# Optimization experiments

Hardware: AMD Instinct MI355X
Metric: run time of the kernel (lower is better)

## Reference

```python
import jax, jax.numpy as jnp
import numpy as np

N, E, D, K = 32768, 16384, 4, 8          # nodes, hyperedges, edges/node, nodes/edge
IN_DIM, OUT_DIM, EDGE_DIM, NUM_HEADS = 128, 128, 64, 8


def setup_inputs() -> dict:
    key = jax.random.key(0)
    ks = jax.random.split(key, 16)
    s_in = 1.0 / np.sqrt(IN_DIM)
    s_out = 1.0 / np.sqrt(OUT_DIM)
    s_edge = 1.0 / np.sqrt(EDGE_DIM)
    return {
        "x": jax.random.normal(ks[0], (N, IN_DIM), jnp.float32),
        "edge_attr": jax.random.normal(ks[1], (E, EDGE_DIM), jnp.float32),
        "node_edges": jax.random.randint(ks[2], (N, D), 0, E),   # hyperedges containing each node
        "edge_nodes": jax.random.randint(ks[3], (E, K), 0, N),   # nodes inside each hyperedge
        "W_lin": jax.random.normal(ks[4], (OUT_DIM, IN_DIM), jnp.float32) * s_in,
        "W_edge": jax.random.normal(ks[5], (OUT_DIM, EDGE_DIM), jnp.float32) * s_edge,
        "Wq": jax.random.normal(ks[6], (OUT_DIM, OUT_DIM), jnp.float32) * s_out,
        "Wk": jax.random.normal(ks[7], (OUT_DIM, OUT_DIM), jnp.float32) * s_out,
        "Wv": jax.random.normal(ks[8], (OUT_DIM, OUT_DIM), jnp.float32) * s_out,
        "bq": jnp.zeros((OUT_DIM,), jnp.float32),
        "bk": jnp.zeros((OUT_DIM,), jnp.float32),
        "bv": jnp.zeros((OUT_DIM,), jnp.float32),
        "Wo": jax.random.normal(ks[9], (OUT_DIM, OUT_DIM), jnp.float32) * s_out,
        "bo": jnp.zeros((OUT_DIM,), jnp.float32),
    }


def reference(x, edge_attr, node_edges, edge_nodes,
              W_lin, W_edge, Wq, Wk, Wv, bq, bk, bv, Wo, bo):
    n, out_dim = x.shape[0], W_lin.shape[0]
    hd = out_dim // NUM_HEADS
    L = node_edges.shape[1] * edge_nodes.shape[1]  # D*K keys per node

    Wh = x @ W_lin.T                               # [N, out]
    We = edge_attr @ W_edge.T                      # [E, out]

    u_idx = edge_nodes[node_edges]                 # [N, D, K] neighbor node ids
    vals = Wh[u_idx]                               # [N, D, K, out]
    keys = vals + We[node_edges][:, :, None, :]    # key = Wh[u] + We[e]
    keys = keys.reshape(n, L, out_dim)
    vals = vals.reshape(n, L, out_dim)

    # torch nn.MultiheadAttention: single query per node (query = Wh[v])
    q = (Wh @ Wq.T + bq).reshape(n, NUM_HEADS, hd)
    k = (keys @ Wk.T + bk).reshape(n, L, NUM_HEADS, hd)
    v = (vals @ Wv.T + bv).reshape(n, L, NUM_HEADS, hd)

    scores = jnp.einsum('nhd,nlhd->nhl', q, k) / jnp.sqrt(jnp.asarray(hd, q.dtype))
    attn = jax.nn.softmax(scores, axis=-1)         # [N, H, L]
    ctx = jnp.einsum('nhl,nlhd->nhd', attn, v).reshape(n, out_dim)
    out = ctx @ Wo.T + bo
    return jax.nn.relu(out)
```

## Files before the change

### kernel.cpp

```cpp
#include <hip/hip_runtime.h>

#define N_NODES 32768
#define N_EDGES 16384
#define DEG 4
#define KPE 8
#define DIM 128
#define EDIM 64

typedef float f32x4 __attribute__((ext_vector_type(4)));
typedef __bf16 bf16x8 __attribute__((ext_vector_type(8)));
typedef __bf16 bf16x2 __attribute__((ext_vector_type(2)));
typedef unsigned short u16x8 __attribute__((ext_vector_type(8)));
typedef unsigned int u32;

static __device__ __forceinline__ unsigned short f2bf(float f) {
  union { float f; unsigned int u; } v; v.f = f;
  unsigned int r = (v.u + 0x7FFFu + ((v.u >> 16) & 1u)) >> 16;
  return (unsigned short)r;
}
static __device__ __forceinline__ float bflo(unsigned int v) {
  union { unsigned int u; float f; } x; x.u = v << 16; return x.f;
}
static __device__ __forceinline__ float bfhi(unsigned int v) {
  union { unsigned int u; float f; } x; x.u = v & 0xffff0000u; return x.f;
}

#if __has_builtin(__builtin_amdgcn_fdot2_f32_bf16)
static __device__ __forceinline__ float dot2bf(unsigned int a, unsigned int b, float c) {
  return __builtin_amdgcn_fdot2_f32_bf16(
      __builtin_bit_cast(bf16x2, a), __builtin_bit_cast(bf16x2, b), c, false);
}
#else
static __device__ __forceinline__ float dot2bf(unsigned int a, unsigned int b, float c) {
  c = fmaf(bflo(a), bflo(b), c);
  return fmaf(bfhi(a), bfhi(b), c);
}
#endif

__global__ __launch_bounds__(256) void wprep_kernel(
    const float* __restrict__ Wq, const float* __restrict__ Wk,
    const float* __restrict__ Wv, const float* __restrict__ Wlin,
    const float* __restrict__ Wedge, const float* __restrict__ Wo,
    unsigned short* __restrict__ CW, unsigned short* __restrict__ CWE,
    unsigned short* __restrict__ Wob)
{
  int id = blockIdx.x * 256 + threadIdx.x;
  if (id < 384 * 128) {
    int j = id >> 7, i = id & 127;
    const float* wrow; float scale = 1.0f;
    if (j < 128)      { wrow = Wq + j * 128; scale = 0.25f; }
    else if (j < 256) { wrow = Wk + (j - 128) * 128; }
    else              { wrow = Wv + (j - 256) * 128; }
    float s = 0.f;
    #pragma unroll 8
    for (int m = 0; m < 128; ++m) s += wrow[m] * Wlin[m * 128 + i];
    CW[id] = f2bf(s * scale);
  } else if (id < 384 * 128 + 128 * 64) {
    int id2 = id - 384 * 128; int j = id2 >> 6, t = id2 & 63;
    float s = 0.f;
    #pragma unroll 8
    for (int m = 0; m < 128; ++m) s += Wk[j * 128 + m] * Wedge[m * 64 + t];
    CWE[id2] = f2bf(s);
  } else if (id < 384 * 128 + 128 * 64 + 128 * 128) {
    int id3 = id - (384 * 128 + 128 * 64);
    Wob[id3] = f2bf(Wo[id3]);
  }
}

__global__ __launch_bounds__(256) void g1_kernel(
    const float* __restrict__ x, const unsigned short* __restrict__ CW,
    const float* __restrict__ bq, const float* __restrict__ bv,
    unsigned short* __restrict__ qb, unsigned short* __restrict__ Kb,
    unsigned short* __restrict__ Vb)
{
  const int wave = threadIdx.x >> 6, lane = threadIdx.x & 63;
  const int r16 = lane & 15, quad = lane >> 4;
  const int m0 = blockIdx.x * 64 + wave * 16;

  u16x8 av[4];
  const float* arow = x + (size_t)(m0 + r16) * DIM + quad * 8;
  #pragma unroll
  for (int kk = 0; kk < 4; ++kk) {
    float4 a0 = *(const float4*)(arow + kk * 32);
    float4 a1 = *(const float4*)(arow + kk * 32 + 4);
    u16x8 au;
    au[0] = f2bf(a0.x); au[1] = f2bf(a0.y); au[2] = f2bf(a0.z); au[3] = f2bf(a0.w);
    au[4] = f2bf(a1.x); au[5] = f2bf(a1.y); au[6] = f2bf(a1.z); au[7] = f2bf(a1.w);
    av[kk] = au;
  }

  #pragma unroll
  for (int g = 0; g < 6; ++g) {
    f32x4 acc[4];
    const f32x4 z = {0.f, 0.f, 0.f, 0.f};
    acc[0] = z; acc[1] = z; acc[2] = z; acc[3] = z;
    #pragma unroll
    for (int kk = 0; kk < 4; ++kk) {
      #pragma unroll
      for (int s = 0; s < 4; ++s) {
        u16x8 bu = *(const u16x8*)(CW + (size_t)(g * 64 + s * 16 + r16) * DIM + kk * 32 + quad * 8);
        acc[s] = __builtin_amdgcn_mfma_f32_16x16x32_bf16(
            __builtin_bit_cast(bf16x8, av[kk]), __builtin_bit_cast(bf16x8, bu), acc[s], 0, 0, 0);
      }
    }
    const int arr = g >> 1;
    const int colbase = (g & 1) * 64;
    unsigned short* dst = arr == 0 ? qb : (arr == 1 ? Kb : Vb);
    #pragma unroll
    for (int s = 0; s < 4; ++s) {
      int j = colbase + s * 16 + r16;
      float bias = arr == 0 ? 0.25f * bq[j] : (arr == 2 ? bv[j] : 0.f);
      #pragma unroll
      for (int r = 0; r < 4; ++r) {
        int m = m0 + quad * 4 + r;
        dst[(size_t)m * DIM + j] = f2bf(acc[s][r] + bias);
      }
    }
  }
}

__global__ __launch_bounds__(256) void g2_kernel(
    const float* __restrict__ ea, const unsigned short* __restrict__ CWE,
    const float* __restrict__ bk, unsigned short* __restrict__ WeKb)
{
  const int wave = threadIdx.x >> 6, lane = threadIdx.x & 63;
  const int r16 = lane & 15, quad = lane >> 4;
  const int m0 = blockIdx.x * 64 + wave * 16;
  const int n0 = blockIdx.y * 64;

  f32x4 acc[4];
  const f32x4 z = {0.f, 0.f, 0.f, 0.f};
  acc[0] = z; acc[1] = z; acc[2] = z; acc[3] = z;

  const float* arow = ea + (size_t)(m0 + r16) * EDIM + quad * 8;
  #pragma unroll
  for (int kk = 0; kk < 2; ++kk) {
    float4 a0 = *(const float4*)(arow + kk * 32);
    float4 a1 = *(const float4*)(arow + kk * 32 + 4);
    u16x8 au;
    au[0] = f2bf(a0.x); au[1] = f2bf(a0.y); au[2] = f2bf(a0.z); au[3] = f2bf(a0.w);
    au[4] = f2bf(a1.x); au[5] = f2bf(a1.y); au[6] = f2bf(a1.z); au[7] = f2bf(a1.w);
    bf16x8 av = __builtin_bit_cast(bf16x8, au);
    #pragma unroll
    for (int s = 0; s < 4; ++s) {
      u16x8 bu = *(const u16x8*)(CWE + (size_t)(n0 + s * 16 + r16) * EDIM + kk * 32 + quad * 8);
      acc[s] = __builtin_amdgcn_mfma_f32_16x16x32_bf16(
          av, __builtin_bit_cast(bf16x8, bu), acc[s], 0, 0, 0);
    }
  }

  #pragma unroll
  for (int s = 0; s < 4; ++s) {
    int j = n0 + s * 16 + r16;
    float bias = bk[j];
    #pragma unroll
    for (int r = 0; r < 4; ++r) {
      int m = m0 + quad * 4 + r;
      WeKb[(size_t)m * DIM + j] = f2bf(acc[s][r] + bias);
    }
  }
}

__global__ __launch_bounds__(64, 2) void attn_kernel(
    const unsigned short* __restrict__ qb, const unsigned short* __restrict__ Kb,
    const unsigned short* __restrict__ Vb, const unsigned short* __restrict__ WeKb,
    const int* __restrict__ nedges, const int* __restrict__ enodes,
    unsigned short* __restrict__ ctxb)
{
  __shared__ __align__(16) unsigned short ldsV[32][128];
  __shared__ __align__(16) float ldsP[8][36];
  const int lane = threadIdx.x;
  const int n = blockIdx.x;
  const int l = lane & 31, half = lane >> 5;
  const int j = l >> 3, lo8 = l & 7;
  const int c0 = lane * 2;
  const int h = lane >> 3;

  int4 e4 = *(const int4*)(nedges + (size_t)n * DEG);
  int e = (j & 2) ? ((j & 1) ? e4.w : e4.z) : ((j & 1) ? e4.y : e4.x);
  int u = enodes[(size_t)e * KPE + lo8];

  int4 m0 = *(const int4*)(enodes + (size_t)e4.x * KPE);
  int4 m1 = *(const int4*)(enodes + (size_t)e4.x * KPE + 4);
  int4 m2 = *(const int4*)(enodes + (size_t)e4.y * KPE);
  int4 m3 = *(const int4*)(enodes + (size_t)e4.y * KPE + 4);
  int4 m4 = *(const int4*)(enodes + (size_t)e4.z * KPE);
  int4 m5 = *(const int4*)(enodes + (size_t)e4.z * KPE + 4);
  int4 m6 = *(const int4*)(enodes + (size_t)e4.w * KPE);
  int4 m7 = *(const int4*)(enodes + (size_t)e4.w * KPE + 4);

  const uint4* qp = (const uint4*)(qb + (size_t)n * DIM + half * 64);
  const uint4* kp = (const uint4*)(Kb + (size_t)u * DIM + half * 64);
  const uint4* ep = (const uint4*)(WeKb + (size_t)e * DIM + half * 64);
  uint4 qv[8], kv[8], ev[8];
  #pragma unroll
  for (int ch = 0; ch < 8; ++ch) qv[ch] = qp[ch];
  #pragma unroll
  for (int ch = 0; ch < 8; ++ch) kv[ch] = kp[ch];
  #pragma unroll
  for (int ch = 0; ch < 8; ++ch) ev[ch] = ep[ch];

#define STAGE_V(t, node) do {                                                   \
    const u32* gp_ = (const u32*)(Vb + (size_t)(node) * DIM) + lane;            \
    __builtin_amdgcn_global_load_lds(                                           \
        (const __attribute__((address_space(1))) u32*)gp_,                      \
        (__attribute__((address_space(3))) u32*)&ldsV[t][0], 4, 0, 0);          \
  } while (0)
  STAGE_V(0,  m0.x); STAGE_V(1,  m0.y); STAGE_V(2,  m0.z); STAGE_V(3,  m0.w);
  STAGE_V(4,  m1.x); STAGE_V(5,  m1.y); STAGE_V(6,  m1.z); STAGE_V(7,  m1.w);
  STAGE_V(8,  m2.x); STAGE_V(9,  m2.y); STAGE_V(10, m2.z); STAGE_V(11, m2.w);
  STAGE_V(12, m3.x); STAGE_V(13, m3.y); STAGE_V(14, m3.z); STAGE_V(15, m3.w);
  STAGE_V(16, m4.x); STAGE_V(17, m4.y); STAGE_V(18, m4.z); STAGE_V(19, m4.w);
  STAGE_V(20, m5.x); STAGE_V(21, m5.y); STAGE_V(22, m5.z); STAGE_V(23, m5.w);
  STAGE_V(24, m6.x); STAGE_V(25, m6.y); STAGE_V(26, m6.z); STAGE_V(27, m6.w);
  STAGE_V(28, m7.x); STAGE_V(29, m7.y); STAGE_V(30, m7.z); STAGE_V(31, m7.w);
#undef STAGE_V

  float s[4] = {0.f, 0.f, 0.f, 0.f};
  #pragma unroll
  for (int ch = 0; ch < 8; ++ch) {
    const int hi = ch >> 1;
    float t = s[hi];
    t = dot2bf(qv[ch].x, kv[ch].x, t); t = dot2bf(qv[ch].x, ev[ch].x, t);
    t = dot2bf(qv[ch].y, kv[ch].y, t); t = dot2bf(qv[ch].y, ev[ch].y, t);
    t = dot2bf(qv[ch].z, kv[ch].z, t); t = dot2bf(qv[ch].z, ev[ch].z, t);
    t = dot2bf(qv[ch].w, kv[ch].w, t); t = dot2bf(qv[ch].w, ev[ch].w, t);
    s[hi] = t;
  }

  #pragma unroll
  for (int hi = 0; hi < 4; ++hi) {
    float vmax = s[hi];
    #pragma unroll
    for (int off = 16; off >= 1; off >>= 1)
      vmax = fmaxf(vmax, __shfl_xor(vmax, off, 32));
    float ex = __expf(s[hi] - vmax);
    float sum = ex;
    #pragma unroll
    for (int off = 16; off >= 1; off >>= 1)
      sum += __shfl_xor(sum, off, 32);
    ldsP[half * 4 + hi][l] = ex / sum;
  }
  __syncthreads();

  float a0 = 0.f, a1 = 0.f;
  #pragma unroll
  for (int t = 0; t < 8; ++t) {
    float4 p4 = *(const float4*)&ldsP[h][t * 4];
    u32 v0 = *(const u32*)&ldsV[t * 4 + 0][c0];
    u32 v1 = *(const u32*)&ldsV[t * 4 + 1][c0];
    u32 v2 = *(const u32*)&ldsV[t * 4 + 2][c0];
    u32 v3 = *(const u32*)&ldsV[t * 4 + 3][c0];
    a0 = fmaf(p4.x, bflo(v0), a0); a1 = fmaf(p4.x, bfhi(v0), a1);
    a0 = fmaf(p4.y, bflo(v1), a0); a1 = fmaf(p4.y, bfhi(v1), a1);
    a0 = fmaf(p4.z, bflo(v2), a0); a1 = fmaf(p4.z, bfhi(v2), a1);
    a0 = fmaf(p4.w, bflo(v3), a0); a1 = fmaf(p4.w, bfhi(v3), a1);
  }
  unsigned int pk = (unsigned int)f2bf(a0) | ((unsigned int)f2bf(a1) << 16);
  *(unsigned int*)(ctxb + (size_t)n * DIM + c0) = pk;
}

__global__ __launch_bounds__(256) void g4_kernel(
    const unsigned short* __restrict__ ctxb, const unsigned short* __restrict__ Wob,
    const float* __restrict__ bo, float* __restrict__ out)
{
  const int wave = threadIdx.x >> 6, lane = threadIdx.x & 63;
  const int r16 = lane & 15, quad = lane >> 4;
  const int m0 = blockIdx.x * 64 + wave * 16;
  const int n0 = blockIdx.y * 64;

  f32x4 acc[4];
  const f32x4 z = {0.f, 0.f, 0.f, 0.f};
  acc[0] = z; acc[1] = z; acc[2] = z; acc[3] = z;

  #pragma unroll
  for (int kk = 0; kk < 4; ++kk) {
    u16x8 au = *(const u16x8*)(ctxb + (size_t)(m0 + r16) * DIM + kk * 32 + quad * 8);
    bf16x8 av = __builtin_bit_cast(bf16x8, au);
    #pragma unroll
    for (int s = 0; s < 4; ++s) {
      u16x8 bu = *(const u16x8*)(Wob + (size_t)(n0 + s * 16 + r16) * DIM + kk * 32 + quad * 8);
      acc[s] = __builtin_amdgcn_mfma_f32_16x16x32_bf16(
          av, __builtin_bit_cast(bf16x8, bu), acc[s], 0, 0, 0);
    }
  }

  #pragma unroll
  for (int s = 0; s < 4; ++s) {
    int j = n0 + s * 16 + r16;
    float bias = bo[j];
    #pragma unroll
    for (int r = 0; r < 4; ++r) {
      int m = m0 + quad * 4 + r;
      float v = acc[s][r] + bias;
      out[(size_t)m * DIM + j] = v > 0.f ? v : 0.f;
    }
  }
}

extern "C" void kernel_launch(void* const* d_in, const int* in_sizes, int n_in,
                              void* d_out, int out_size, void* d_ws, size_t ws_size,
                              hipStream_t stream)
{
  const float* x     = (const float*)d_in[0];
  const float* ea    = (const float*)d_in[1];
  const int* nedges  = (const int*)d_in[2];
  const int* enodes  = (const int*)d_in[3];
  const float* Wlin  = (const float*)d_in[4];
  const float* Wedge = (const float*)d_in[5];
  const float* Wq    = (const float*)d_in[6];
  const float* Wk    = (const float*)d_in[7];
  const float* Wv    = (const float*)d_in[8];
  const float* bq    = (const float*)d_in[9];
  const float* bk    = (const float*)d_in[10];
  const float* bv    = (const float*)d_in[11];
  const float* Wo    = (const float*)d_in[12];
  const float* bo    = (const float*)d_in[13];
  float* out = (float*)d_out;

  unsigned short* wsp = (unsigned short*)d_ws;
  unsigned short* CW   = wsp;  wsp += 384 * 128;
  unsigned short* CWE  = wsp;  wsp += 128 * 64;
  unsigned short* Wob  = wsp;  wsp += 128 * 128;
  unsigned short* qb   = wsp;  wsp += (size_t)N_NODES * DIM;
  unsigned short* Kb   = wsp;  wsp += (size_t)N_NODES * DIM;
  unsigned short* Vb   = wsp;  wsp += (size_t)N_NODES * DIM;
  unsigned short* WeKb = wsp;  wsp += (size_t)N_EDGES * DIM;
  unsigned short* ctxb = wsp;  wsp += (size_t)N_NODES * DIM;

  wprep_kernel<<<dim3(288), dim3(256), 0, stream>>>(Wq, Wk, Wv, Wlin, Wedge, Wo, CW, CWE, Wob);
  g1_kernel<<<dim3(512), dim3(256), 0, stream>>>(x, CW, bq, bv, qb, Kb, Vb);
  g2_kernel<<<dim3(256, 2), dim3(256), 0, stream>>>(ea, CWE, bk, WeKb);
  attn_kernel<<<dim3(32768), dim3(64), 0, stream>>>(qb, Kb, Vb, WeKb, nedges, enodes, ctxb);
  g4_kernel<<<dim3(512, 2), dim3(256), 0, stream>>>(ctxb, Wob, bo, out);
}
```

Baseline: 215.5 us.

## Merge node and edge projection GEMMs and stage K/We rows into LDS

Merges the two projection GEMM launches (node Q/K/V and edge We·K) into one grid with block-index dispatch, removing a kernel launch and letting the two run concurrently. In the attention kernel, the per-lane direct global loads of K and We rows are replaced by async global_load_lds staging of all 32 K rows, 4 We rows and 32 V rows into padded (272-byte stride) LDS buffers, then read from LDS after a barrier. This aims to issue the gathers as coalesced bulk transfers and avoid bank conflicts. In exchange it raises LDS use per block, which may reduce occupancy, and adds an extra barrier.

```diff
diff --git a/kernel.cpp b/kernel.cpp
--- a/kernel.cpp
+++ b/kernel.cpp
@@ -67,96 +67,90 @@
   }
 }
 
-__global__ __launch_bounds__(256) void g1_kernel(
+__global__ __launch_bounds__(256) void g12_kernel(
     const float* __restrict__ x, const unsigned short* __restrict__ CW,
     const float* __restrict__ bq, const float* __restrict__ bv,
     unsigned short* __restrict__ qb, unsigned short* __restrict__ Kb,
-    unsigned short* __restrict__ Vb)
+    unsigned short* __restrict__ Vb,
+    const float* __restrict__ ea, const unsigned short* __restrict__ CWE,
+    const float* __restrict__ bk, unsigned short* __restrict__ WeKb)
 {
   const int wave = threadIdx.x >> 6, lane = threadIdx.x & 63;
   const int r16 = lane & 15, quad = lane >> 4;
-  const int m0 = blockIdx.x * 64 + wave * 16;
-
-  u16x8 av[4];
-  const float* arow = x + (size_t)(m0 + r16) * DIM + quad * 8;
-  #pragma unroll
-  for (int kk = 0; kk < 4; ++kk) {
-    float4 a0 = *(const float4*)(arow + kk * 32);
-    float4 a1 = *(const float4*)(arow + kk * 32 + 4);
-    u16x8 au;
-    au[0] = f2bf(a0.x); au[1] = f2bf(a0.y); au[2] = f2bf(a0.z); au[3] = f2bf(a0.w);
-    au[4] = f2bf(a1.x); au[5] = f2bf(a1.y); au[6] = f2bf(a1.z); au[7] = f2bf(a1.w);
-    av[kk] = au;
-  }
-
-  #pragma unroll
-  for (int g = 0; g < 6; ++g) {
+
+  if (blockIdx.x < 512) {
+    const int m0 = blockIdx.x * 64 + wave * 16;
+    u16x8 av[4];
+    const float* arow = x + (size_t)(m0 + r16) * DIM + quad * 8;
+    #pragma unroll
+    for (int kk = 0; kk < 4; ++kk) {
+      float4 a0 = *(const float4*)(arow + kk * 32);
+      float4 a1 = *(const float4*)(arow + kk * 32 + 4);
+      u16x8 au;
+      au[0] = f2bf(a0.x); au[1] = f2bf(a0.y); au[2] = f2bf(a0.z); au[3] = f2bf(a0.w);
+      au[4] = f2bf(a1.x); au[5] = f2bf(a1.y); au[6] = f2bf(a1.z); au[7] = f2bf(a1.w);
+      av[kk] = au;
+    }
+    #pragma unroll
+    for (int g = 0; g < 6; ++g) {
+      f32x4 acc[4];
+      const f32x4 z = {0.f, 0.f, 0.f, 0.f};
+      acc[0] = z; acc[1] = z; acc[2] = z; acc[3] = z;
+      #pragma unroll
+      for (int kk = 0; kk < 4; ++kk) {
+        #pragma unroll
+        for (int s = 0; s < 4; ++s) {
+          u16x8 bu = *(const u16x8*)(CW + (size_t)(g * 64 + s * 16 + r16) * DIM + kk * 32 + quad * 8);
+          acc[s] = __builtin_amdgcn_mfma_f32_16x16x32_bf16(
+              __builtin_bit_cast(bf16x8, av[kk]), __builtin_bit_cast(bf16x8, bu), acc[s], 0, 0, 0);
+        }
+      }
+      const int arr = g >> 1;
+      const int colbase = (g & 1) * 64;
+      unsigned short* dst = arr == 0 ? qb : (arr == 1 ? Kb : Vb);
+      #pragma unroll
+      for (int s = 0; s < 4; ++s) {
+        int j = colbase + s * 16 + r16;
+        float bias = arr == 0 ? 0.25f * bq[j] : (arr == 2 ? bv[j] : 0.f);
+        #pragma unroll
+        for (int r = 0; r < 4; ++r) {
+          int m = m0 + quad * 4 + r;
+          dst[(size_t)m * DIM + j] = f2bf(acc[s][r] + bias);
+        }
+      }
+    }
+  } else {
+    const int idx = blockIdx.x - 512;
+    const int m0 = (idx >> 1) * 64 + wave * 16;
+    const int n0 = (idx & 1) * 64;
     f32x4 acc[4];
     const f32x4 z = {0.f, 0.f, 0.f, 0.f};
     acc[0] = z; acc[1] = z; acc[2] = z; acc[3] = z;
-    #pragma unroll
-    for (int kk = 0; kk < 4; ++kk) {
+    const float* arow = ea + (size_t)(m0 + r16) * EDIM + quad * 8;
+    #pragma unroll
+    for (int kk = 0; kk < 2; ++kk) {
+      float4 a0 = *(const float4*)(arow + kk * 32);
+      float4 a1 = *(const float4*)(arow + kk * 32 + 4);
+      u16x8 au;
+      au[0] = f2bf(a0.x); au[1] = f2bf(a0.y); au[2] = f2bf(a0.z); au[3] = f2bf(a0.w);
+      au[4] = f2bf(a1.x); au[5] = f2bf(a1.y); au[6] = f2bf(a1.z); au[7] = f2bf(a1.w);
+      bf16x8 av = __builtin_bit_cast(bf16x8, au);
       #pragma unroll
       for (int s = 0; s < 4; ++s) {
-        u16x8 bu = *(const u16x8*)(CW + (size_t)(g * 64 + s * 16 + r16) * DIM + kk * 32 + quad * 8);
+        u16x8 bu = *(const u16x8*)(CWE + (size_t)(n0 + s * 16 + r16) * EDIM + kk * 32 + quad * 8);
         acc[s] = __builtin_amdgcn_mfma_f32_16x16x32_bf16(
-            __builtin_bit_cast(bf16x8, av[kk]), __builtin_bit_cast(bf16x8, bu), acc[s], 0, 0, 0);
+            av, __builtin_bit_cast(bf16x8, bu), acc[s], 0, 0, 0);
       }
     }
-    const int arr = g >> 1;
-    const int colbase = (g & 1) * 64;
-    unsigned short* dst = arr == 0 ? qb : (arr == 1 ? Kb : Vb);
     #pragma unroll
     for (int s = 0; s < 4; ++s) {
-      int j = colbase + s * 16 + r16;
-      float bias = arr == 0 ? 0.25f * bq[j] : (arr == 2 ? bv[j] : 0.f);
+      int j = n0 + s * 16 + r16;
+      float bias = bk[j];
       #pragma unroll
       for (int r = 0; r < 4; ++r) {
         int m = m0 + quad * 4 + r;
-        dst[(size_t)m * DIM + j] = f2bf(acc[s][r] + bias);
+        WeKb[(size_t)m * DIM + j] = f2bf(acc[s][r] + bias);
       }
-    }
-  }
-}
-
-__global__ __launch_bounds__(256) void g2_kernel(
-    const float* __restrict__ ea, const unsigned short* __restrict__ CWE,
-    const float* __restrict__ bk, unsigned short* __restrict__ WeKb)
-{
-  const int wave = threadIdx.x >> 6, lane = threadIdx.x & 63;
-  const int r16 = lane & 15, quad = lane >> 4;
-  const int m0 = blockIdx.x * 64 + wave * 16;
-  const int n0 = blockIdx.y * 64;
-
-  f32x4 acc[4];
-  const f32x4 z = {0.f, 0.f, 0.f, 0.f};
-  acc[0] = z; acc[1] = z; acc[2] = z; acc[3] = z;
-
-  const float* arow = ea + (size_t)(m0 + r16) * EDIM + quad * 8;
-  #pragma unroll
-  for (int kk = 0; kk < 2; ++kk) {
-    float4 a0 = *(const float4*)(arow + kk * 32);
-    float4 a1 = *(const float4*)(arow + kk * 32 + 4);
-    u16x8 au;
-    au[0] = f2bf(a0.x); au[1] = f2bf(a0.y); au[2] = f2bf(a0.z); au[3] = f2bf(a0.w);
-    au[4] = f2bf(a1.x); au[5] = f2bf(a1.y); au[6] = f2bf(a1.z); au[7] = f2bf(a1.w);
-    bf16x8 av = __builtin_bit_cast(bf16x8, au);
-    #pragma unroll
-    for (int s = 0; s < 4; ++s) {
-      u16x8 bu = *(const u16x8*)(CWE + (size_t)(n0 + s * 16 + r16) * EDIM + kk * 32 + quad * 8);
-      acc[s] = __builtin_amdgcn_mfma_f32_16x16x32_bf16(
-          av, __builtin_bit_cast(bf16x8, bu), acc[s], 0, 0, 0);
-    }
-  }
-
-  #pragma unroll
-  for (int s = 0; s < 4; ++s) {
-    int j = n0 + s * 16 + r16;
-    float bias = bk[j];
-    #pragma unroll
-    for (int r = 0; r < 4; ++r) {
-      int m = m0 + quad * 4 + r;
-      WeKb[(size_t)m * DIM + j] = f2bf(acc[s][r] + bias);
     }
   }
 }
@@ -167,19 +161,16 @@
     const int* __restrict__ nedges, const int* __restrict__ enodes,
     unsigned short* __restrict__ ctxb)
 {
-  __shared__ __align__(16) unsigned short ldsV[32][128];
+  __shared__ __align__(16) unsigned char ldsK[32 * 272];
+  __shared__ __align__(16) unsigned char ldsV[32 * 272];
+  __shared__ __align__(16) unsigned char ldsE[4 * 272];
   __shared__ __align__(16) float ldsP[8][36];
   const int lane = threadIdx.x;
   const int n = blockIdx.x;
   const int l = lane & 31, half = lane >> 5;
-  const int j = l >> 3, lo8 = l & 7;
-  const int c0 = lane * 2;
   const int h = lane >> 3;
 
   int4 e4 = *(const int4*)(nedges + (size_t)n * DEG);
-  int e = (j & 2) ? ((j & 1) ? e4.w : e4.z) : ((j & 1) ? e4.y : e4.x);
-  int u = enodes[(size_t)e * KPE + lo8];
-
   int4 m0 = *(const int4*)(enodes + (size_t)e4.x * KPE);
   int4 m1 = *(const int4*)(enodes + (size_t)e4.x * KPE + 4);
   int4 m2 = *(const int4*)(enodes + (size_t)e4.y * KPE);
@@ -190,41 +181,67 @@
   int4 m7 = *(const int4*)(enodes + (size_t)e4.w * KPE + 4);
 
   const uint4* qp = (const uint4*)(qb + (size_t)n * DIM + half * 64);
-  const uint4* kp = (const uint4*)(Kb + (size_t)u * DIM + half * 64);
-  const uint4* ep = (const uint4*)(WeKb + (size_t)e * DIM + half * 64);
-  uint4 qv[8], kv[8], ev[8];
+  uint4 qv[8];
   #pragma unroll
   for (int ch = 0; ch < 8; ++ch) qv[ch] = qp[ch];
-  #pragma unroll
-  for (int ch = 0; ch < 8; ++ch) kv[ch] = kp[ch];
-  #pragma unroll
-  for (int ch = 0; ch < 8; ++ch) ev[ch] = ep[ch];
-
-#define STAGE_V(t, node) do {                                                   \
-    const u32* gp_ = (const u32*)(Vb + (size_t)(node) * DIM) + lane;            \
+
+#define STAGE(ldsdst, table, row) do {                                          \
+    const u32* gp_ = (const u32*)((table) + (size_t)(row) * DIM) + lane;        \
     __builtin_amdgcn_global_load_lds(                                           \
         (const __attribute__((address_space(1))) u32*)gp_,                      \
-        (__attribute__((address_space(3))) u32*)&ldsV[t][0], 4, 0, 0);          \
+        (__attribute__((address_space(3))) u32*)(ldsdst), 4, 0, 0);             \
   } while (0)
-  STAGE_V(0,  m0.x); STAGE_V(1,  m0.y); STAGE_V(2,  m0.z); STAGE_V(3,  m0.w);
-  STAGE_V(4,  m1.x); STAGE_V(5,  m1.y); STAGE_V(6,  m1.z); STAGE_V(7,  m1.w);
-  STAGE_V(8,  m2.x); STAGE_V(9,  m2.y); STAGE_V(10, m2.z); STAGE_V(11, m2.w);
-  STAGE_V(12, m3.x); STAGE_V(13, m3.y); STAGE_V(14, m3.z); STAGE_V(15, m3.w);
-  STAGE_V(16, m4.x); STAGE_V(17, m4.y); STAGE_V(18, m4.z); STAGE_V(19, m4.w);
-  STAGE_V(20, m5.x); STAGE_V(21, m5.y); STAGE_V(22, m5.z); STAGE_V(23, m5.w);
-  STAGE_V(24, m6.x); STAGE_V(25, m6.y); STAGE_V(26, m6.z); STAGE_V(27, m6.w);
-  STAGE_V(28, m7.x); STAGE_V(29, m7.y); STAGE_V(30, m7.z); STAGE_V(31, m7.w);
-#undef STAGE_V
-
+  STAGE(ldsK + 0  * 272, Kb, m0.x); STAGE(ldsK + 1  * 272, Kb, m0.y);
+  STAGE(ldsK + 2  * 272, Kb, m0.z); STAGE(ldsK + 3  * 272, Kb, m0.w);
+  STAGE(ldsK + 4  * 272, Kb, m1.x); STAGE(ldsK + 5  * 272, Kb, m1.y);
+  STAGE(ldsK + 6  * 272, Kb, m1.z); STAGE(ldsK + 7  * 272, Kb, m1.w);
+  STAGE(ldsK + 8  * 272, Kb, m2.x); STAGE(ldsK + 9  * 272, Kb, m2.y);
+  STAGE(ldsK + 10 * 272, Kb, m2.z); STAGE(ldsK + 11 * 272, Kb, m2.w);
+  STAGE(ldsK + 12 * 272, Kb, m3.x); STAGE(ldsK + 13 * 272, Kb, m3.y);
+  STAGE(ldsK + 14 * 272, Kb, m3.z); STAGE(ldsK + 15 * 272, Kb, m3.w);
+  STAGE(ldsK + 16 * 272, Kb, m4.x); STAGE(ldsK + 17 * 272, Kb, m4.y);
+  STAGE(ldsK + 18 * 272, Kb, m4.z); STAGE(ldsK + 19 * 272, Kb, m4.w);
+  STAGE(ldsK + 20 * 272, Kb, m5.x); STAGE(ldsK + 21 * 272, Kb, m5.y);
+  STAGE(ldsK + 22 * 272, Kb, m5.z); STAGE(ldsK + 23 * 272, Kb, m5.w);
+  STAGE(ldsK + 24 * 272, Kb, m6.x); STAGE(ldsK + 25 * 272, Kb, m6.y);
+  STAGE(ldsK + 26 * 272, Kb, m6.z); STAGE(ldsK + 27 * 272, Kb, m6.w);
+  STAGE(ldsK + 28 * 272, Kb, m7.x); STAGE(ldsK + 29 * 272, Kb, m7.y);
+  STAGE(ldsK + 30 * 272, Kb, m7.z); STAGE(ldsK + 31 * 272, Kb, m7.w);
+  STAGE(ldsE + 0 * 272, WeKb, e4.x); STAGE(ldsE + 1 * 272, WeKb, e4.y);
+  STAGE(ldsE + 2 * 272, WeKb, e4.z); STAGE(ldsE + 3 * 272, WeKb, e4.w);
+  STAGE(ldsV + 0  * 272, Vb, m0.x); STAGE(ldsV + 1  * 272, Vb, m0.y);
+  STAGE(ldsV + 2  * 272, Vb, m0.z); STAGE(ldsV + 3  * 272, Vb, m0.w);
+  STAGE(ldsV + 4  * 272, Vb, m1.x); STAGE(ldsV + 5  * 272, Vb, m1.y);
+  STAGE(ldsV + 6  * 272, Vb, m1.z); STAGE(ldsV + 7  * 272, Vb, m1.w);
+  STAGE(ldsV + 8  * 272, Vb, m2.x); STAGE(ldsV + 9  * 272, Vb, m2.y);
+  STAGE(ldsV + 10 * 272, Vb, m2.z); STAGE(ldsV + 11 * 272, Vb, m2.w);
+  STAGE(ldsV + 12 * 272, Vb, m3.x); STAGE(ldsV + 13 * 272, Vb, m3.y);
+  STAGE(ldsV + 14 * 272, Vb, m3.z); STAGE(ldsV + 15 * 272, Vb, m3.w);
+  STAGE(ldsV + 16 * 272, Vb, m4.x); STAGE(ldsV + 17 * 272, Vb, m4.y);
+  STAGE(ldsV + 18 * 272, Vb, m4.z); STAGE(ldsV + 19 * 272, Vb, m4.w);
+  STAGE(ldsV + 20 * 272, Vb, m5.x); STAGE(ldsV + 21 * 272, Vb, m5.y);
+  STAGE(ldsV + 22 * 272, Vb, m5.z); STAGE(ldsV + 23 * 272, Vb, m5.w);
+  STAGE(ldsV + 24 * 272, Vb, m6.x); STAGE(ldsV + 25 * 272, Vb, m6.y);
+  STAGE(ldsV + 26 * 272, Vb, m6.z); STAGE(ldsV + 27 * 272, Vb, m6.w);
+  STAGE(ldsV + 28 * 272, Vb, m7.x); STAGE(ldsV + 29 * 272, Vb, m7.y);
+  STAGE(ldsV + 30 * 272, Vb, m7.z); STAGE(ldsV + 31 * 272, Vb, m7.w);
+#undef STAGE
+
+  __syncthreads();
+
+  const unsigned char* krow = ldsK + l * 272 + half * 128;
+  const unsigned char* erow = ldsE + (l >> 3) * 272 + half * 128;
   float s[4] = {0.f, 0.f, 0.f, 0.f};
   #pragma unroll
   for (int ch = 0; ch < 8; ++ch) {
+    uint4 kc = *(const uint4*)(krow + ch * 16);
+    uint4 ec = *(const uint4*)(erow + ch * 16);
     const int hi = ch >> 1;
     float t = s[hi];
-    t = dot2bf(qv[ch].x, kv[ch].x, t); t = dot2bf(qv[ch].x, ev[ch].x, t);
-    t = dot2bf(qv[ch].y, kv[ch].y, t); t = dot2bf(qv[ch].y, ev[ch].y, t);
-    t = dot2bf(qv[ch].z, kv[ch].z, t); t = dot2bf(qv[ch].z, ev[ch].z, t);
-    t = dot2bf(qv[ch].w, kv[ch].w, t); t = dot2bf(qv[ch].w, ev[ch].w, t);
+    t = dot2bf(qv[ch].x, kc.x, t); t = dot2bf(qv[ch].x, ec.x, t);
+    t = dot2bf(qv[ch].y, kc.y, t); t = dot2bf(qv[ch].y, ec.y, t);
+    t = dot2bf(qv[ch].z, kc.z, t); t = dot2bf(qv[ch].z, ec.z, t);
+    t = dot2bf(qv[ch].w, kc.w, t); t = dot2bf(qv[ch].w, ec.w, t);
     s[hi] = t;
   }
 
@@ -247,17 +264,17 @@
   #pragma unroll
   for (int t = 0; t < 8; ++t) {
     float4 p4 = *(const float4*)&ldsP[h][t * 4];
-    u32 v0 = *(const u32*)&ldsV[t * 4 + 0][c0];
-    u32 v1 = *(const u32*)&ldsV[t * 4 + 1][c0];
-    u32 v2 = *(const u32*)&ldsV[t * 4 + 2][c0];
-    u32 v3 = *(const u32*)&ldsV[t * 4 + 3][c0];
+    u32 v0 = *(const u32*)(ldsV + (t * 4 + 0) * 272 + lane * 4);
+    u32 v1 = *(const u32*)(ldsV + (t * 4 + 1) * 272 + lane * 4);
+    u32 v2 = *(const u32*)(ldsV + (t * 4 + 2) * 272 + lane * 4);
+    u32 v3 = *(const u32*)(ldsV + (t * 4 + 3) * 272 + lane * 4);
     a0 = fmaf(p4.x, bflo(v0), a0); a1 = fmaf(p4.x, bfhi(v0), a1);
     a0 = fmaf(p4.y, bflo(v1), a0); a1 = fmaf(p4.y, bfhi(v1), a1);
     a0 = fmaf(p4.z, bflo(v2), a0); a1 = fmaf(p4.z, bfhi(v2), a1);
     a0 = fmaf(p4.w, bflo(v3), a0); a1 = fmaf(p4.w, bfhi(v3), a1);
   }
   unsigned int pk = (unsigned int)f2bf(a0) | ((unsigned int)f2bf(a1) << 16);
-  *(unsigned int*)(ctxb + (size_t)n * DIM + c0) = pk;
+  *(unsigned int*)(ctxb + (size_t)n * DIM + lane * 2) = pk;
 }
 
 __global__ __launch_bounds__(256) void g4_kernel(
@@ -329,8 +346,7 @@
   unsigned short* ctxb = wsp;  wsp += (size_t)N_NODES * DIM;
 
   wprep_kernel<<<dim3(288), dim3(256), 0, stream>>>(Wq, Wk, Wv, Wlin, Wedge, Wo, CW, CWE, Wob);
-  g1_kernel<<<dim3(512), dim3(256), 0, stream>>>(x, CW, bq, bv, qb, Kb, Vb);
-  g2_kernel<<<dim3(256, 2), dim3(256), 0, stream>>>(ea, CWE, bk, WeKb);
+  g12_kernel<<<dim3(1024), dim3(256), 0, stream>>>(x, CW, bq, bv, qb, Kb, Vb, ea, CWE, bk, WeKb);
   attn_kernel<<<dim3(32768), dim3(64), 0, stream>>>(qb, Kb, Vb, WeKb, nedges, enodes, ctxb);
   g4_kernel<<<dim3(512, 2), dim3(256), 0, stream>>>(ctxb, Wob, bo, out);
 }
```

After: 230.2 us. +6.8%, slower.
